# Optimization experiments

Hardware: AMD Instinct MI355X
Metric: run time of the kernel (lower is better)

## Reference

```python
import jax, jax.numpy as jnp
import numpy as np

B, N, DE, DH, L, DC = 8, 256, 768, 192, 2, 192
NEG = 1e30  # mask_logic constant from the repo


def setup_inputs() -> dict:
    ks = iter(jax.random.split(jax.random.key(0), 32))

    def nrm(shape, s=0.02):
        return jax.random.normal(next(ks), shape, dtype=jnp.float32) * s

    features = jax.random.normal(next(ks), (B, N, DE), dtype=jnp.float32)
    # DAG adjacency: node i attends to a subset of j < i; guarantee edge (i, i-1)
    rnd = jax.random.bernoulli(next(ks), 0.3, (B, N, N))
    tril = jnp.tril(jnp.ones((N, N), jnp.bool_), -1)
    adj = ((rnd & tril[None]) | jnp.eye(N, k=-1, dtype=jnp.bool_)[None]).astype(jnp.float32)
    s_mask = jax.random.bernoulli(next(ks), 0.5, (B, N, N)).astype(jnp.float32)
    s_mask_onehot = jnp.stack([1.0 - s_mask, s_mask], axis=-1)  # unused in forward
    lengths = jnp.full((B,), N, dtype=jnp.int32)  # unused (nodal_att_type=None)
    return dict(
        features=features, adj=adj, s_mask=s_mask,
        s_mask_onehot=s_mask_onehot, lengths=lengths,
        fc1_w=nrm((DE, DH)), fc1_b=jnp.zeros((DH,), jnp.float32),
        gat_w=nrm((L, 2 * DH)), gat_b=jnp.zeros((L,), jnp.float32),
        wr0=nrm((L, DH, DH)), wr1=nrm((L, DH, DH)),
        gruc_wih=nrm((L, 3 * DH, DH)), gruc_whh=nrm((L, 3 * DH, DH)),
        gruc_bih=jnp.zeros((L, 3 * DH), jnp.float32),
        gruc_bhh=jnp.zeros((L, 3 * DH), jnp.float32),
        grup_wih=nrm((L, 3 * DH, DH)), grup_whh=nrm((L, 3 * DH, DH)),
        grup_bih=jnp.zeros((L, 3 * DH), jnp.float32),
        grup_bhh=jnp.zeros((L, 3 * DH), jnp.float32),
        mlp_w0=nrm((DH * (L + 1), DH)), mlp_b0=jnp.zeros((DH,), jnp.float32),
        mlp_w1=nrm((DH, DH)), mlp_b1=jnp.zeros((DH,), jnp.float32),
        mlp_w2=nrm((DH, DC)), mlp_b2=jnp.zeros((DC,), jnp.float32),
    )


def _gru(x, h, wih, whh, bih, bhh):
    # torch.nn.GRUCell math
    gi = x @ wih.T + bih
    gh = h @ whh.T + bhh
    ir, iz, inn = jnp.split(gi, 3, axis=-1)
    hr, hz, hn = jnp.split(gh, 3, axis=-1)
    r = jax.nn.sigmoid(ir + hr)
    z = jax.nn.sigmoid(iz + hz)
    n = jnp.tanh(inn + r * hn)
    return (1.0 - z) * n + z * h


def _layer(Hl, adj, s_mask, gat_w, gat_b, wr0, wr1, cw, cp):
    # One DAG layer: sequential scan over nodes. Carry holds the relation-
    # projected value buffers V0=H1@Wr0^T, V1=H1@Wr1^T and per-node key
    # scores Ksc=H1@wk (rows >= i are zero and masked out), which is
    # mathematically identical to the torch code that re-projects the
    # growing H1 every step.
    wq, wk = gat_w[:DH], gat_w[DH:]
    pos = jnp.arange(N)

    def step(carry, xs):
        V0, V1, Ksc = carry
        i, x_i, adj_i, sm_i = xs  # x_i:(B,DH) adj_i,sm_i:(B,N)
        score = (x_i @ wq)[:, None] + Ksc + gat_b          # (B,N)
        mask = (pos < i)[None, :] & (adj_i > 0.5)          # ragged :i slice
        alpha = jnp.where(mask, score, score - NEG)        # mask_logic
        attn = jax.nn.softmax(alpha, axis=-1)              # masked -> exactly 0
        Vrel = V0 * sm_i[..., None] + V1 * (1.0 - sm_i[..., None])
        M = jnp.einsum('bn,bnd->bd', attn, Vrel)
        M = jnp.where(i > 0, M, 0.0)                       # node 0: no context
        C = _gru(x_i, M, *cw)
        P = _gru(M, x_i, *cp)
        Hnew = C + P
        V0 = V0.at[:, i, :].set(Hnew @ wr0.T)
        V1 = V1.at[:, i, :].set(Hnew @ wr1.T)
        Ksc = Ksc.at[:, i].set(Hnew @ wk)
        attn_out = jnp.where(i > 0, attn, 0.0)             # adjB row 0 is zeros
        return (V0, V1, Ksc), (Hnew, attn_out)

    z3 = jnp.zeros((B, N, DH), jnp.float32)
    carry0 = (z3, z3, jnp.zeros((B, N), jnp.float32))
    xs = (pos, Hl.transpose(1, 0, 2), adj.transpose(1, 0, 2), s_mask.transpose(1, 0, 2))
    _, (Hseq, Aseq) = jax.lax.scan(step, carry0, xs)
    return Hseq.transpose(1, 0, 2), Aseq.transpose(1, 0, 2)  # (B,N,DH),(B,N,N)


def reference(features, adj, s_mask, s_mask_onehot, lengths,
              fc1_w, fc1_b, gat_w, gat_b, wr0, wr1,
              gruc_wih, gruc_whh, gruc_bih, gruc_bhh,
              grup_wih, grup_whh, grup_bih, grup_bhh,
              mlp_w0, mlp_b0, mlp_w1, mlp_b1, mlp_w2, mlp_b2):
    Hl = jax.nn.relu(features @ fc1_w + fc1_b)  # H0
    Hs, As = [Hl], []
    for l in range(L):
        cw = (gruc_wih[l], gruc_whh[l], gruc_bih[l], gruc_bhh[l])
        cp = (grup_wih[l], grup_whh[l], grup_bih[l], grup_bhh[l])
        Hl, Al = _layer(Hl, adj, s_mask, gat_w[l], gat_b[l], wr0[l], wr1[l], cw, cp)
        Hs.append(Hl)
        As.append(Al)
    H = jnp.concatenate(Hs, axis=2)  # (B,N,DH*(L+1))
    # nodal_att_type=None => attentive_node_features is identity
    h = jax.nn.relu(H @ mlp_w0 + mlp_b0)
    h = jax.nn.relu(h @ mlp_w1 + mlp_b1)  # mlp_layers-1 = 1 extra block
    logits = h @ mlp_w2 + mlp_b2          # dropout: eval-mode identity
    return logits, jnp.stack(As, axis=1)  # (B,N,DC), (B,L,N,N)
```

## Files before the change

kernel.cpp:

```cpp
#include <hip/hip_runtime.h>
#include <stdint.h>

#define B_  8
#define N_  256
#define DH_ 192
#define L_  2
#define G3  576
#define G6  1152
#define NW  4
#define DS  48
#define KD  24
#define GC  288
#define MPSZ (8 * NW * DH_ * 3)
#define KDSZ (8 * NW)
#define STH 10001
#define STP 20001
#define SPK 50000
#define SF1 50001
#define SF2 50002
#define SDN 60001

typedef unsigned long long u64;

__device__ __forceinline__ float bflo(uint32_t u) { return __uint_as_float(u << 16); }
__device__ __forceinline__ float bfhi(uint32_t u) { return __uint_as_float(u & 0xffff0000u); }
__device__ __forceinline__ uint32_t f2bf(float f) {
    uint32_t x = __float_as_uint(f);
    x += 0x7fffu + ((x >> 16) & 1u);
    return x >> 16;
}
__device__ __forceinline__ float sigm(float x)  { return 1.f / (1.f + __expf(-x)); }
__device__ __forceinline__ float tanhf_(float x){ return 1.f - 2.f / (1.f + __expf(2.f * x)); }
__device__ __forceinline__ u64 packvs(float v, int st) {
    return ((u64)(uint32_t)st << 32) | __float_as_uint(v);
}
__device__ __forceinline__ u64 agload(const u64* p) {
    return __hip_atomic_load(p, __ATOMIC_RELAXED, __HIP_MEMORY_SCOPE_AGENT);
}
__device__ __forceinline__ void agstore(u64* p, u64 v) {
    __hip_atomic_store(p, v, __ATOMIC_RELAXED, __HIP_MEMORY_SCOPE_AGENT);
}
__device__ __forceinline__ float u2f(u64 v) { return __uint_as_float((uint32_t)v); }

__device__ __forceinline__ void wg_barrier() {
    asm volatile("s_waitcnt lgkmcnt(0)" ::: "memory");
    __builtin_amdgcn_s_barrier();
    asm volatile("" ::: "memory");
}

struct ScanSm {
    uint4 Wr4s[12 * DH_];
    float sA0[2][N_], sA1[2][N_], sKsc[N_];
    float sAdjN[N_], sSmN[N_];
    float sPre[6 * DS], sXv[DS];
    float sM[DH_], su0[DS], su1[DS], sGc[GC], sHn[DS];
    float sRl[DH_], sP0l[DH_], sP1l[DH_];
    float sRedS[2][8], sSaved[8], sSavedA[2], sSavedS[2];
};
struct WorkSm {
    float sX[DH_];
    float sPv[GC];
};
struct PrologSm {
    float sA[8][768];
    float sRed[3][8][192];
};
struct MlpSm {
    float sH[8][576];
    float sRed[3][8][192];
    float sT[8][192];
};
union SmemAll { ScanSm s; WorkSm w; PrologSm p; MlpSm m; };

__device__ void prepack_slice(int idx,
    const float* __restrict__ wr0, const float* __restrict__ wr1,
    const float* __restrict__ c_wih, const float* __restrict__ c_whh,
    const float* __restrict__ c_bih, const float* __restrict__ c_bhh,
    const float* __restrict__ p_wih, const float* __restrict__ p_whh,
    const float* __restrict__ p_bih, const float* __restrict__ p_bhh,
    float* __restrict__ WpreT, uint32_t* __restrict__ W4,
    uint32_t* __restrict__ Wr4, uint32_t* __restrict__ Wp4w,
    float* __restrict__ biasPre, float* __restrict__ gbx)
{
    for (int l = 0; l < L_; ++l) {
        const float* cwih = c_wih + l * G3 * DH_;
        const float* cwhh = c_whh + l * G3 * DH_;
        const float* pwih = p_wih + l * G3 * DH_;
        const float* pwhh = p_whh + l * G3 * DH_;
        if (l == 0) {
            int k = idx / G6, r = idx - k * G6;
            float w = (r < G3) ? cwih[r * DH_ + k] : pwhh[(r - G3) * DH_ + k];
            WpreT[k * G6 + r] = w;
        }
        if (idx < NW * 27648) {
            int w = idx / 27648, pos = idx % 27648;
            int p4 = pos / 1152, rem = pos % 1152;
            int c2 = rem >> 2, s = rem & 3;
            int p = 4 * p4 + s;
            int j = c2 / DS, dd = c2 % DS;
            int c = 192 * j + DS * w + dd;
            float w0 = (c < G3) ? cwhh[c * DH_ + 2 * p]     : pwih[(c - G3) * DH_ + 2 * p];
            float w1 = (c < G3) ? cwhh[c * DH_ + 2 * p + 1] : pwih[(c - G3) * DH_ + 2 * p + 1];
            W4[l * NW * 27648 + idx] = f2bf(w0) | (f2bf(w1) << 16);
            if (l == 1) {
                int r = c;
                float v0 = (r < G3) ? cwih[r * DH_ + 2 * p]     : pwhh[(r - G3) * DH_ + 2 * p];
                float v1 = (r < G3) ? cwih[r * DH_ + 2 * p + 1] : pwhh[(r - G3) * DH_ + 2 * p + 1];
                Wp4w[idx] = f2bf(v0) | (f2bf(v1) << 16);
            }
        }
        if (idx < NW * 9216) {
            int w = idx / 9216, pos = idx % 9216;
            int kq = pos / 768, rem = pos % 768;
            int d = rem >> 2, s = rem & 3;
            int k = DS * w + 4 * kq + s;
            Wr4[l * NW * 9216 + idx] =
                f2bf(wr0[l * DH_ * DH_ + d * DH_ + k]) |
                (f2bf(wr1[l * DH_ * DH_ + d * DH_ + k]) << 16);
        }
        if (idx < G6) {
            float base = (idx < G3) ? c_bih[l * G3 + idx] : p_bhh[l * G3 + idx - G3];
            float fold = 0.f;
            if (idx < 384)                    fold = c_bhh[l * G3 + idx];
            else if (idx >= G3 && idx < 960)  fold = p_bih[l * G3 + idx - G3];
            biasPre[l * G6 + idx] = base + fold;
        }
        if (idx < 384) {
            gbx[l * 384 + idx] = (idx < DH_) ? c_bhh[l * G3 + 384 + idx]
                                             : p_bih[l * G3 + 384 + (idx - DH_)];
        }
    }
}

__device__ void flag_sync(u64* flags, int wgid, int t, int stamp)
{
    __threadfence();
    __syncthreads();
    if (t == 0) agstore(&flags[wgid], packvs(0.f, stamp));
    if (t < 96) {
        while ((uint32_t)(agload(&flags[t]) >> 32) != (uint32_t)stamp) {}
    }
    __syncthreads();
    __threadfence();
    __syncthreads();
}

__device__ void prologue(char* smem, int wgid, int t,
    const float* __restrict__ features, const float* __restrict__ fc1_w,
    const float* __restrict__ fc1_b, const float* __restrict__ WpreT,
    const float* __restrict__ biasPre,
    float* __restrict__ Hcat, float* __restrict__ PREg, u64* __restrict__ Fp)
{
    PrologSm* P = (PrologSm*)smem;
    const int c = t % 192, kg = t / 192;
    for (int tt = wgid; tt < 256; tt += 96) {
        const int r0 = tt * 8;
        for (int q = t; q < 1536; q += 576) {
            int r = q / 192, c4 = q % 192;
            *(float4*)&P->sA[r][4 * c4] = *(const float4*)(features + (size_t)(r0 + r) * 768 + 4 * c4);
        }
        __syncthreads();
        {
            const float* bp = fc1_w + (size_t)(kg * 256) * 192 + c;
            float acc[8] = {0.f, 0.f, 0.f, 0.f, 0.f, 0.f, 0.f, 0.f};
            #pragma unroll 8
            for (int kk = 0; kk < 256; ++kk) {
                float bv = bp[(size_t)kk * 192];
                #pragma unroll
                for (int rr = 0; rr < 8; ++rr) acc[rr] += P->sA[rr][kg * 256 + kk] * bv;
            }
            #pragma unroll
            for (int rr = 0; rr < 8; ++rr) P->sRed[kg][rr][c] = acc[rr];
        }
        __syncthreads();
        if (t < 192) {
            float bv = fc1_b[t];
            #pragma unroll
            for (int rr = 0; rr < 8; ++rr) {
                float v = P->sRed[0][rr][t] + P->sRed[1][rr][t] + P->sRed[2][rr][t] + bv;
                Hcat[(size_t)(r0 + rr) * G3 + t] = fmaxf(v, 0.f);
            }
        }
        __syncthreads();
    }
    flag_sync(Fp + 96, wgid, t, SF1);
    {
        const float bpa = biasPre[t], bpb = biasPre[576 + t];
        for (int tt = wgid; tt < 256; tt += 96) {
            const int r0 = tt * 8;
            for (int q = t; q < 384; q += 576) {
                int r = q / 48, c4 = q % 48;
                *(float4*)&P->sA[r][4 * c4] = *(const float4*)(Hcat + (size_t)(r0 + r) * G3 + 4 * c4);
            }
            __syncthreads();
            {
                const float* b0 = WpreT + t;
                float a0[8] = {0.f,0.f,0.f,0.f,0.f,0.f,0.f,0.f};
                float a1[8] = {0.f,0.f,0.f,0.f,0.f,0.f,0.f,0.f};
                #pragma unroll 4
                for (int k = 0; k < 192; ++k) {
                    float bva = b0[(size_t)k * G6];
                    float bvb = b0[(size_t)k * G6 + 576];
                    #pragma unroll
                    for (int rr = 0; rr < 8; ++rr) {
                        float av = P->sA[rr][k];
                        a0[rr] += av * bva; a1[rr] += av * bvb;
                    }
                }
                #pragma unroll
                for (int rr = 0; rr < 8; ++rr) {
                    PREg[(size_t)(r0 + rr) * G6 + t]       = a0[rr] + bpa;
                    PREg[(size_t)(r0 + rr) * G6 + 576 + t] = a1[rr] + bpb;
                }
            }
            __syncthreads();
        }
    }
    flag_sync(Fp + 192, wgid, t, SF2);
}

__device__ void mlp_tail(char* smem, int wgid, int t,
    const float* __restrict__ Hcat,
    const float* __restrict__ mw0, const float* __restrict__ mb0,
    const float* __restrict__ mw1, const float* __restrict__ mb1,
    const float* __restrict__ mw2, const float* __restrict__ mb2,
    float* __restrict__ out, u64* __restrict__ Fd)
{
    if (t < 64) {
        while ((uint32_t)(agload(&Fd[t]) >> 32) != (uint32_t)SDN)
            __builtin_amdgcn_s_sleep(2);
    }
    __syncthreads();
    __threadfence();
    __syncthreads();
    MlpSm* M = (MlpSm*)smem;
    const int c = t % 192, kg = t / 192;
    for (int tt = wgid; tt < 256; tt += 96) {
        const int r0 = tt * 8;
        for (int q = t; q < 1152; q += 576) {
            int r = q / 144, c4 = q % 144;
            *(float4*)&M->sH[r][4 * c4] = *(const float4*)(Hcat + (size_t)(r0 + r) * G3 + 4 * c4);
        }
        __syncthreads();
        {
            const float* bp = mw0 + (size_t)(kg * 192) * 192 + c;
            float acc[8] = {0.f,0.f,0.f,0.f,0.f,0.f,0.f,0.f};
            #pragma unroll 8
            for (int kk = 0; kk < 192; ++kk) {
                float bv = bp[(size_t)kk * 192];
                #pragma unroll
                for (int rr = 0; rr < 8; ++rr) acc[rr] += M->sH[rr][kg * 192 + kk] * bv;
            }
            #pragma unroll
            for (int rr = 0; rr < 8; ++rr) M->sRed[kg][rr][c] = acc[rr];
        }
        __syncthreads();
        if (t < 192) {
            float bv = mb0[t];
            #pragma unroll
            for (int rr = 0; rr < 8; ++rr)
                M->sT[rr][t] = fmaxf(M->sRed[0][rr][t] + M->sRed[1][rr][t] + M->sRed[2][rr][t] + bv, 0.f);
        }
        __syncthreads();
        {
            const float* bp = mw1 + (size_t)(kg * 64) * 192 + c;
            float acc[8] = {0.f,0.f,0.f,0.f,0.f,0.f,0.f,0.f};
            #pragma unroll 8
            for (int kk = 0; kk < 64; ++kk) {
                float bv = bp[(size_t)kk * 192];
                #pragma unroll
                for (int rr = 0; rr < 8; ++rr) acc[rr] += M->sT[rr][kg * 64 + kk] * bv;
            }
            #pragma unroll
            for (int rr = 0; rr < 8; ++rr) M->sRed[kg][rr][c] = acc[rr];
        }
        __syncthreads();
        if (t < 192) {
            float bv = mb1[t];
            #pragma unroll
            for (int rr = 0; rr < 8; ++rr)
                M->sH[rr][t] = fmaxf(M->sRed[0][rr][t] + M->sRed[1][rr][t] + M->sRed[2][rr][t] + bv, 0.f);
        }
        __syncthreads();
        {
            const float* bp = mw2 + (size_t)(kg * 64) * 192 + c;
            float acc[8] = {0.f,0.f,0.f,0.f,0.f,0.f,0.f,0.f};
            #pragma unroll 8
            for (int kk = 0; kk < 64; ++kk) {
                float bv = bp[(size_t)kk * 192];
                #pragma unroll
                for (int rr = 0; rr < 8; ++rr) acc[rr] += M->sH[rr][kg * 64 + kk] * bv;
            }
            #pragma unroll
            for (int rr = 0; rr < 8; ++rr) M->sRed[kg][rr][c] = acc[rr];
        }
        __syncthreads();
        if (t < 192) {
            float bv = mb2[t];
            #pragma unroll
            for (int rr = 0; rr < 8; ++rr)
                out[(size_t)(r0 + rr) * 192 + t] =
                    M->sRed[0][rr][t] + M->sRed[1][rr][t] + M->sRed[2][rr][t] + bv;
        }
        __syncthreads();
    }
}

template<int ISL2>
__device__ void scan_body(
    ScanSm* S, int b, int w, int t,
    const float* __restrict__ xin, float* __restrict__ hout,
    const float* __restrict__ PREg, const float* __restrict__ adj,
    const float* __restrict__ smask,
    const uint32_t* __restrict__ W4l, const uint32_t* __restrict__ Wr4l,
    const float* __restrict__ gbxl, const float* __restrict__ gatwl,
    uint32_t* __restrict__ Hw, u64* __restrict__ MPsl, u64* __restrict__ Kdl,
    u64* __restrict__ HcW, const u64* __restrict__ HcR,
    const u64* __restrict__ PREcR,
    float* __restrict__ AsB, int sbase)
{
    const int lane = t & 63, wave = t >> 6;
    const int dg0 = w * DS;
    const float* adjB = adj   + (size_t)b * N_ * N_;
    const float* smB  = smask + (size_t)b * N_ * N_;
    const int fi = b * NW;
    const int cB4 = t >> 1, khB4 = t & 1;
    const int w1 = (w + 1) & 3, w2 = (w + 2) & 3, w3 = (w + 3) & 3;

    {
        uint32_t* wr = (uint32_t*)S->Wr4s;
        for (int q = t; q < 9216; q += 576) wr[q] = Wr4l[q];
    }
    uint4 wreg[12];
    {
        const uint4* W4v = (const uint4*)W4l;
        #pragma unroll
        for (int p4 = 0; p4 < 12; ++p4) wreg[p4] = W4v[(12 * khB4 + p4) * GC + cB4];
    }
    float wkv = 0.f, g2b = 0.f, g5b = 0.f;
    if (t < DS) { wkv = gatwl[DH_ + dg0 + t]; g2b = gbxl[dg0 + t]; g5b = gbxl[DH_ + dg0 + t]; }
    if (t < N_) { S->sKsc[t] = 0.f; S->sA0[1][t] = 0.f; S->sA1[1][t] = 0.f; }
    if (t < DS) { S->su0[t] = 0.f; S->su1[t] = 0.f; }
    if (t < 8)  S->sRedS[1][t] = 0.f;
    if (w == 0 && t < N_) AsB[t] = 0.f;

    if (!ISL2) {
        if (t < DS) {
            const float* pre = PREg + (size_t)(b * N_) * G6 + dg0 + t;
            S->sPre[t] = pre[0]; S->sPre[DS + t] = pre[192]; S->sPre[2 * DS + t] = pre[384];
            S->sPre[3 * DS + t] = pre[576]; S->sPre[4 * DS + t] = pre[768]; S->sPre[5 * DS + t] = pre[960];
            S->sXv[t] = xin[(size_t)(b * N_) * G3 + dg0 + t];
        }
        for (int q = t; q < 128; q += 576) {
            if (q < 64)  *(float4*)&S->sAdjN[4 * q] = *(const float4*)(adjB + N_ + 4 * q);
            else { int q2 = q - 64; *(float4*)&S->sSmN[4 * q2] = *(const float4*)(smB + N_ + 4 * q2); }
        }
    } else {
        for (int q = t; q < 320; q += 576) {
            if (q < 64)       *(float4*)&S->sAdjN[4 * q] = *(const float4*)(adjB + N_ + 4 * q);
            else if (q < 128) { int q2 = q - 64;  *(float4*)&S->sSmN[4 * q2] = *(const float4*)(smB + N_ + 4 * q2); }
            else if (q < 176) {
                int d = q - 128;
                const u64* p = HcR + ((size_t)(b * N_) * NW + w) * DS + d;
                u64 v; do { v = agload(p); } while ((uint32_t)(v >> 32) != (uint32_t)STH);
                S->sXv[d] = __uint_as_float((uint32_t)v);
            } else {
                int qq = q - 176;
                const u64* p = PREcR + ((size_t)(b * N_) * NW + w) * 144 + qq;
                u64 v; do { v = agload(p); } while ((uint32_t)(v >> 32) != (uint32_t)STP);
                uint32_t pl = (uint32_t)v;
                S->sPre[2 * qq] = bflo(pl); S->sPre[2 * qq + 1] = bfhi(pl);
            }
        }
    }
    __syncthreads();
    {
        float hn = 0.f;
        if (t < DS) {
            float xv = S->sXv[t];
            float r1 = sigm(S->sPre[t]), z1 = sigm(S->sPre[DS + t]);
            float n1 = tanhf_(S->sPre[2 * DS + t] + r1 * g2b);
            float Cv = (1.f - z1) * n1;
            float r2 = sigm(S->sPre[3 * DS + t]), z2 = sigm(S->sPre[4 * DS + t]);
            float n2 = tanhf_(g5b + r2 * S->sPre[5 * DS + t]);
            hn = Cv + (1.f - z2) * n2 + z2 * xv;
            S->sHn[t] = hn;
            hout[(size_t)(b * N_) * G3 + dg0 + t] = hn;
            if (!ISL2) HcW[((size_t)(b * N_) * NW + w) * DS + t] = packvs(hn, STH);
        }
        if (t == 0) { S->sSavedA[1] = S->sAdjN[0]; S->sSavedS[1] = S->sSmN[0]; }
        if (wave == 0) {
            float v = hn * wkv;
            #pragma unroll
            for (int o = 32; o; o >>= 1) v += __shfl_xor(v, o);
            if (lane == 0) { S->sSaved[6] = v; agstore(&Kdl[fi + w], packvs(v, sbase)); }
        }
    }
    __syncthreads();
    if (t < KD) Hw[(size_t)t * N_] = f2bf(S->sHn[2 * t]) | (f2bf(S->sHn[2 * t + 1]) << 16);
    __syncthreads();

    for (int i = 1; i < N_; ++i) {
        const int row = b * N_ + i;
        const int stamp = sbase + i;
        const int pp = i & 1, pn = pp ^ 1;

        if (t < DH_) {
            float rr = 0.f, p0 = 0.f, p1 = 0.f;
            #pragma unroll 4
            for (int kq = 0; kq < 12; ++kq) {
                uint4 wv = S->Wr4s[kq * DH_ + t];
                const int k0 = 4 * kq;
                float lo, hi;
                lo = bflo(wv.x); hi = bfhi(wv.x);
                rr = fmaf(S->su0[k0 + 0], lo, rr); rr = fmaf(S->su1[k0 + 0], hi, rr);
                p0 = fmaf(S->sHn[k0 + 0], lo, p0); p1 = fmaf(S->sHn[k0 + 0], hi, p1);
                lo = bflo(wv.y); hi = bfhi(wv.y);
                rr = fmaf(S->su0[k0 + 1], lo, rr); rr = fmaf(S->su1[k0 + 1], hi, rr);
                p0 = fmaf(S->sHn[k0 + 1], lo, p0); p1 = fmaf(S->sHn[k0 + 1], hi, p1);
                lo = bflo(wv.z); hi = bfhi(wv.z);
                rr = fmaf(S->su0[k0 + 2], lo, rr); rr = fmaf(S->su1[k0 + 2], hi, rr);
                p0 = fmaf(S->sHn[k0 + 2], lo, p0); p1 = fmaf(S->sHn[k0 + 2], hi, p1);
                lo = bflo(wv.w); hi = bfhi(wv.w);
                rr = fmaf(S->su0[k0 + 3], lo, rr); rr = fmaf(S->su1[k0 + 3], hi, rr);
                p0 = fmaf(S->sHn[k0 + 3], lo, p0); p1 = fmaf(S->sHn[k0 + 3], hi, p1);
            }
            S->sRl[t] = rr; S->sP0l[t] = p0; S->sP1l[t] = p1;
            u64* base = &MPsl[(size_t)pp * MPSZ + ((size_t)(fi + w) * DH_ + t) * 3];
            agstore(base + 0, packvs(rr, stamp));
            agstore(base + 1, packvs(p0, stamp));
            agstore(base + 2, packvs(p1, stamp));
        } else if (t >= 384) {
            const int u = t - 384;
            const int inx = (i + 1 < N_) ? i + 1 : N_ - 1;
            if (!ISL2) {
                for (int qq = u; qq < 212; qq += 192) {
                    if (qq < 64)
                        *(float4*)&S->sAdjN[4 * qq] = *(const float4*)(adjB + (size_t)inx * N_ + 4 * qq);
                    else if (qq < 128) { int q2 = qq - 64;
                        *(float4*)&S->sSmN[4 * q2] = *(const float4*)(smB + (size_t)inx * N_ + 4 * q2); }
                    else if (qq < 140) { int q2 = qq - 128;
                        *(float4*)&S->sXv[4 * q2] = *(const float4*)(xin + (size_t)row * G3 + dg0 + 4 * q2); }
                    else { int q2 = qq - 140; int g = q2 / 12, o = q2 - 12 * g;
                        *(float4*)&S->sPre[g * DS + 4 * o] =
                            *(const float4*)(PREg + (size_t)row * G6 + g * DH_ + dg0 + 4 * o); }
                }
            } else {
                for (int qq = u; qq < 320; qq += 192) {
                    if (qq < 64)
                        *(float4*)&S->sAdjN[4 * qq] = *(const float4*)(adjB + (size_t)inx * N_ + 4 * qq);
                    else if (qq < 128) { int q2 = qq - 64;
                        *(float4*)&S->sSmN[4 * q2] = *(const float4*)(smB + (size_t)inx * N_ + 4 * q2); }
                    else if (qq < 176) {
                        int d = qq - 128;
                        const u64* p = HcR + ((size_t)row * NW + w) * DS + d;
                        u64 v; do { v = agload(p); } while ((uint32_t)(v >> 32) != (uint32_t)(STH + i));
                        S->sXv[d] = __uint_as_float((uint32_t)v);
                    } else {
                        int q2 = qq - 176;
                        const u64* p = PREcR + ((size_t)row * NW + w) * 144 + q2;
                        u64 v; do { v = agload(p); } while ((uint32_t)(v >> 32) != (uint32_t)(STP + i));
                        uint32_t pl = (uint32_t)v;
                        S->sPre[2 * q2] = bflo(pl); S->sPre[2 * q2 + 1] = bfhi(pl);
                    }
                }
            }
        }
        wg_barrier();

        if (t < N_) {
            float e = 0.f;
            if (t == i) { S->sSavedA[pn] = S->sAdjN[t]; S->sSavedS[pn] = S->sSmN[t]; }
            if (t < i - 1 && S->sAdjN[t] > 0.5f) e = __expf(S->sKsc[t]);
            float b0 = e * S->sSmN[t];
            S->sA0[pn][t] = b0; S->sA1[pn][t] = e - b0;
            float ps = e;
            #pragma unroll
            for (int o = 32; o; o >>= 1) ps += __shfl_xor(ps, o);
            if (lane == 0) S->sRedS[pn][wave] = ps;
        }
        wg_barrier();

        if (t < 384) {
            const int ilim = i - 1;
            const int kd = t >> 4, jp = t & 15;
            const uint32_t* hp = Hw + (size_t)kd * N_;
            float u0l = 0.f, u0h = 0.f, u1l = 0.f, u1h = 0.f;
            int j = jp;
            while (j + 48 < ilim) {
                uint32_t h0 = hp[j], h1 = hp[j + 16], h2 = hp[j + 32], h3 = hp[j + 48];
                float b0, b1;
                b0 = S->sA0[pn][j];      b1 = S->sA1[pn][j];
                u0l = fmaf(b0, bflo(h0), u0l); u0h = fmaf(b0, bfhi(h0), u0h);
                u1l = fmaf(b1, bflo(h0), u1l); u1h = fmaf(b1, bfhi(h0), u1h);
                b0 = S->sA0[pn][j + 16]; b1 = S->sA1[pn][j + 16];
                u0l = fmaf(b0, bflo(h1), u0l); u0h = fmaf(b0, bfhi(h1), u0h);
                u1l = fmaf(b1, bflo(h1), u1l); u1h = fmaf(b1, bfhi(h1), u1h);
                b0 = S->sA0[pn][j + 32]; b1 = S->sA1[pn][j + 32];
                u0l = fmaf(b0, bflo(h2), u0l); u0h = fmaf(b0, bfhi(h2), u0h);
                u1l = fmaf(b1, bflo(h2), u1l); u1h = fmaf(b1, bfhi(h2), u1h);
                b0 = S->sA0[pn][j + 48]; b1 = S->sA1[pn][j + 48];
                u0l = fmaf(b0, bflo(h3), u0l); u0h = fmaf(b0, bfhi(h3), u0h);
                u1l = fmaf(b1, bflo(h3), u1l); u1h = fmaf(b1, bfhi(h3), u1h);
                j += 64;
            }
            for (; j < ilim; j += 16) {
                uint32_t hv = hp[j];
                float b0 = S->sA0[pn][j], b1 = S->sA1[pn][j];
                u0l = fmaf(b0, bflo(hv), u0l); u0h = fmaf(b0, bfhi(hv), u0h);
                u1l = fmaf(b1, bflo(hv), u1l); u1h = fmaf(b1, bfhi(hv), u1h);
            }
            #pragma unroll
            for (int o = 1; o <= 8; o <<= 1) {
                u0l += __shfl_xor(u0l, o); u0h += __shfl_xor(u0h, o);
                u1l += __shfl_xor(u1l, o); u1h += __shfl_xor(u1h, o);
            }
            if (jp == 0) {
                S->su0[2 * kd] = u0l; S->su0[2 * kd + 1] = u0h;
                S->su1[2 * kd] = u1l; S->su1[2 * kd + 1] = u1h;
            }
        } else {
            const int d = t - 384;
            const u64* pA = &MPsl[(size_t)pp * MPSZ + ((size_t)(fi + w1) * DH_ + d) * 3];
            const u64* pB = &MPsl[(size_t)pp * MPSZ + ((size_t)(fi + w2) * DH_ + d) * 3];
            const u64* pC = &MPsl[(size_t)pp * MPSZ + ((size_t)(fi + w3) * DH_ + d) * 3];
            const uint32_t ex = (uint32_t)stamp;
            u64 a0, a1, a2, b0, b1, b2, c0, c1, c2;
            do {
                a0 = agload(pA); a1 = agload(pA + 1); a2 = agload(pA + 2);
                b0 = agload(pB); b1 = agload(pB + 1); b2 = agload(pB + 2);
                c0 = agload(pC); c1 = agload(pC + 1); c2 = agload(pC + 2);
            } while ((uint32_t)(a0 >> 32) != ex || (uint32_t)(a1 >> 32) != ex ||
                     (uint32_t)(a2 >> 32) != ex || (uint32_t)(b0 >> 32) != ex ||
                     (uint32_t)(b1 >> 32) != ex || (uint32_t)(b2 >> 32) != ex ||
                     (uint32_t)(c0 >> 32) != ex || (uint32_t)(c1 >> 32) != ex ||
                     (uint32_t)(c2 >> 32) != ex);
            S->sRl[d]  += u2f(a0) + u2f(b0) + u2f(c0);
            S->sP0l[d] += u2f(a1) + u2f(b1) + u2f(c1);
            S->sP1l[d] += u2f(a2) + u2f(b2) + u2f(c2);
            if (t == 575) {
                const uint32_t ex2 = (uint32_t)(stamp - 1);
                const int kpar = (i - 1) & 1;
                u64 k0, k1, k2;
                u64* q1 = &Kdl[kpar * KDSZ + fi + w1];
                u64* q2 = &Kdl[kpar * KDSZ + fi + w2];
                u64* q3 = &Kdl[kpar * KDSZ + fi + w3];
                do {
                    k0 = agload(q1); k1 = agload(q2); k2 = agload(q3);
                } while ((uint32_t)(k0 >> 32) != ex2 || (uint32_t)(k1 >> 32) != ex2 ||
                         (uint32_t)(k2 >> 32) != ex2);
                float kdot = S->sSaved[6] + u2f(k0) + u2f(k1) + u2f(k2);
                float adj1 = S->sSavedA[pp], sm1 = S->sSavedS[pp];
                float er = __expf(kdot);
                float e1 = (adj1 > 0.5f) ? er : 0.f;
                float Ssum = S->sRedS[pp][0] + S->sRedS[pp][1] + S->sRedS[pp][2]
                           + S->sRedS[pp][3] + S->sRedS[pp][4] + e1;
                S->sKsc[i - 1] = kdot;
                float invS = 1.f / Ssum;
                float e1c0 = e1 * sm1, e1c1 = e1 - e1c0;
                S->sSaved[2] = invS;
                S->sSaved[4] = e1c0; S->sSaved[5] = e1c1;
                S->sA0[pp][i - 1] = e1c0; S->sA1[pp][i - 1] = e1c1;
                float adjn = S->sAdjN[i - 1], smn = S->sSmN[i - 1];
                float en = (adjn > 0.5f) ? er : 0.f;
                float n0 = en * smn;
                S->sA0[pn][i - 1] = n0; S->sA1[pn][i - 1] = en - n0;
                S->sRedS[pn][4] = en;
            }
        }
        wg_barrier();

        if (t < DH_) {
            S->sM[t] = (S->sRl[t] + S->sSaved[4] * S->sP0l[t]
                                  + S->sSaved[5] * S->sP1l[t]) * S->sSaved[2];
        } else if (t < 192 + DS) {
            const int k = t - 192;
            float a0 = S->sA0[pn][i - 1], a1 = S->sA1[pn][i - 1];
            S->su0[k] += a0 * S->sHn[k];
            S->su1[k] += a1 * S->sHn[k];
        } else if (w == 0 && t >= 256 && t < 512) {
            const int j = t - 256;
            AsB[(size_t)i * N_ + j] = (S->sA0[pp][j] + S->sA1[pp][j]) * S->sSaved[2];
        }
        wg_barrier();

        {
            float g = 0.f;
            #pragma unroll
            for (int p4 = 0; p4 < 12; ++p4) {
                const uint4 wv = wreg[p4];
                const int m0 = 8 * (12 * khB4 + p4);
                g = fmaf(S->sM[m0 + 0], bflo(wv.x), g); g = fmaf(S->sM[m0 + 1], bfhi(wv.x), g);
                g = fmaf(S->sM[m0 + 2], bflo(wv.y), g); g = fmaf(S->sM[m0 + 3], bfhi(wv.y), g);
                g = fmaf(S->sM[m0 + 4], bflo(wv.z), g); g = fmaf(S->sM[m0 + 5], bfhi(wv.z), g);
                g = fmaf(S->sM[m0 + 6], bflo(wv.w), g); g = fmaf(S->sM[m0 + 7], bfhi(wv.w), g);
            }
            g += __shfl_xor(g, 1);
            if (khB4 == 0) S->sGc[cB4] = g;
        }
        wg_barrier();

        {
            float hn = 0.f;
            if (t < DS) {
                float Mv = S->sM[dg0 + t];
                float r1 = sigm(S->sPre[t] + S->sGc[t]);
                float z1 = sigm(S->sPre[DS + t] + S->sGc[DS + t]);
                float n1 = tanhf_(S->sPre[2 * DS + t] + r1 * (S->sGc[2 * DS + t] + g2b));
                float Cv = (1.f - z1) * n1 + z1 * Mv;
                float r2 = sigm(S->sGc[3 * DS + t] + S->sPre[3 * DS + t]);
                float z2 = sigm(S->sGc[4 * DS + t] + S->sPre[4 * DS + t]);
                float n2 = tanhf_(S->sGc[5 * DS + t] + g5b + r2 * S->sPre[5 * DS + t]);
                hn = Cv + (1.f - z2) * n2 + z2 * S->sXv[t];
                S->sHn[t] = hn;
                hout[(size_t)row * G3 + dg0 + t] = hn;
                if (!ISL2) HcW[((size_t)row * NW + w) * DS + t] = packvs(hn, STH + i);
            }
            if (wave == 0) {
                float v = hn * wkv;
                #pragma unroll
                for (int o = 32; o; o >>= 1) v += __shfl_xor(v, o);
                if (lane == 0) { S->sSaved[6] = v; agstore(&Kdl[pp * KDSZ + fi + w], packvs(v, stamp)); }
            }
            if (t < KD) Hw[(size_t)t * N_ + i] = f2bf(S->sHn[2 * t]) | (f2bf(S->sHn[2 * t + 1]) << 16);
        }
        wg_barrier();
    }
}

__device__ void worker_body(WorkSm* Wm, int b, int w, int t,
    const uint32_t* __restrict__ Wp4g, const float* __restrict__ bias2,
    const u64* __restrict__ HcR, u64* __restrict__ PREcW)
{
    const int c = t >> 1, kh = t & 1;
    uint4 wpreg[12];
    {
        const uint4* v4 = (const uint4*)Wp4g;
        #pragma unroll
        for (int p4 = 0; p4 < 12; ++p4) wpreg[p4] = v4[(12 * kh + p4) * GC + c];
    }
    float bv = 0.f;
    if (kh == 0) bv = bias2[192 * (c / DS) + w * DS + (c % DS)];
    for (int i = 0; i < N_; ++i) {
        if (t < DH_) {
            const u64* p = HcR + ((size_t)(b * N_ + i) * NW + (t / DS)) * DS + (t % DS);
            u64 v; do { v = agload(p); } while ((uint32_t)(v >> 32) != (uint32_t)(STH + i));
            Wm->sX[t] = __uint_as_float((uint32_t)v);
        }
        wg_barrier();
        {
            float g = 0.f;
            #pragma unroll
            for (int p4 = 0; p4 < 12; ++p4) {
                const uint4 wv = wpreg[p4];
                const int m0 = 8 * (12 * kh + p4);
                g = fmaf(Wm->sX[m0 + 0], bflo(wv.x), g); g = fmaf(Wm->sX[m0 + 1], bfhi(wv.x), g);
                g = fmaf(Wm->sX[m0 + 2], bflo(wv.y), g); g = fmaf(Wm->sX[m0 + 3], bfhi(wv.y), g);
                g = fmaf(Wm->sX[m0 + 4], bflo(wv.z), g); g = fmaf(Wm->sX[m0 + 5], bfhi(wv.z), g);
                g = fmaf(Wm->sX[m0 + 6], bflo(wv.w), g); g = fmaf(Wm->sX[m0 + 7], bfhi(wv.w), g);
            }
            g += __shfl_xor(g, 1);
            if (kh == 0) Wm->sPv[c] = g + bv;
        }
        wg_barrier();
        if (t < 144) {
            u64 v = ((u64)(uint32_t)(STP + i) << 32)
                  | f2bf(Wm->sPv[2 * t]) | (f2bf(Wm->sPv[2 * t + 1]) << 16);
            agstore(&PREcW[((size_t)(b * N_ + i) * NW + w) * 144 + t], v);
        }
        wg_barrier();
    }
}

__global__ __launch_bounds__(576, 1) void pipeline_kernel(
    const float* __restrict__ features, const float* __restrict__ fc1_w,
    const float* __restrict__ fc1_b,
    const float* __restrict__ adj, const float* __restrict__ smask,
    const float* __restrict__ gatw,
    const float* __restrict__ wr0, const float* __restrict__ wr1,
    const float* __restrict__ c_wih, const float* __restrict__ c_whh,
    const float* __restrict__ c_bih, const float* __restrict__ c_bhh,
    const float* __restrict__ p_wih, const float* __restrict__ p_whh,
    const float* __restrict__ p_bih, const float* __restrict__ p_bhh,
    const float* __restrict__ mw0, const float* __restrict__ mb0,
    const float* __restrict__ mw1, const float* __restrict__ mb1,
    const float* __restrict__ mw2, const float* __restrict__ mb2,
    float* __restrict__ Hcat, float* __restrict__ PREg,
    float* __restrict__ WpreT, uint32_t* __restrict__ W4,
    uint32_t* __restrict__ Wr4, uint32_t* __restrict__ Wp4w,
    float* __restrict__ biasPre, float* __restrict__ gbx,
    uint32_t* __restrict__ Hb, u64* __restrict__ MPs, u64* __restrict__ Kd,
    u64* __restrict__ Hc, u64* __restrict__ PREc,
    u64* __restrict__ Fp, u64* __restrict__ Fd,
    float* __restrict__ out)
{
    __shared__ __align__(16) char smem[sizeof(SmemAll)];
    const int blk = blockIdx.x, t = threadIdx.x;
    const int wgid = blk;
    const int b = blk & 7, r12 = blk >> 3;
    const int role = r12 >> 2, w = r12 & 3;

    for (int j = 0; j < 4; ++j) {
        int idx = wgid * 576 + t + 55296 * j;
        prepack_slice(idx, wr0, wr1, c_wih, c_whh, c_bih, c_bhh,
                      p_wih, p_whh, p_bih, p_bhh,
                      WpreT, W4, Wr4, Wp4w, biasPre, gbx);
    }
    flag_sync(Fp, wgid, t, SPK);

    prologue(smem, wgid, t, features, fc1_w, fc1_b, WpreT, biasPre,
             Hcat, PREg, Fp);

    float* As = out + 393216;
    if (role == 0) {
        scan_body<0>((ScanSm*)smem, b, w, t,
            Hcat, Hcat + 192, PREg, adj, smask,
            W4, Wr4, gbx, gatw,
            Hb + (size_t)(b * NW + w) * KD * N_, MPs, Kd,
            Hc, nullptr, nullptr,
            As + (size_t)b * (L_ * N_ * N_), 1);
        __threadfence();
        __syncthreads();
        if (t == 0) agstore(&Fd[b * 8 + w], packvs(0.f, SDN));
    } else if (role == 2) {
        scan_body<1>((ScanSm*)smem, b, w, t,
            nullptr, Hcat + 384, nullptr, adj, smask,
            W4 + NW * 27648, Wr4 + NW * 9216, gbx + 384, gatw + 384,
            Hb + (size_t)(32 + b * NW + w) * KD * N_,
            MPs + (size_t)2 * MPSZ, Kd + 2 * KDSZ,
            nullptr, Hc, PREc,
            As + (size_t)b * (L_ * N_ * N_) + N_ * N_, 30001);
        __threadfence();
        __syncthreads();
        if (t == 0) agstore(&Fd[b * 8 + 4 + w], packvs(0.f, SDN));
    } else {
        worker_body((WorkSm*)smem, b, w, t,
            Wp4w + (size_t)w * 27648, biasPre + G6,
            Hc, PREc);
    }

    mlp_tail(smem, wgid, t, Hcat, mw0, mb0, mw1, mb1, mw2, mb2, out, Fd);
}

extern "C" void kernel_launch(void* const* d_in, const int* in_sizes, int n_in,
                              void* d_out, int out_size, void* d_ws, size_t ws_size,
                              hipStream_t stream)
{
    const float* features = (const float*)d_in[0];
    const float* adj      = (const float*)d_in[1];
    const float* smask    = (const float*)d_in[2];
    const float* fc1_w = (const float*)d_in[5];
    const float* fc1_b = (const float*)d_in[6];
    const float* gat_w = (const float*)d_in[7];
    const float* wr0   = (const float*)d_in[9];
    const float* wr1   = (const float*)d_in[10];
    const float* c_wih = (const float*)d_in[11];
    const float* c_whh = (const float*)d_in[12];
    const float* c_bih = (const float*)d_in[13];
    const float* c_bhh = (const float*)d_in[14];
    const float* p_wih = (const float*)d_in[15];
    const float* p_whh = (const float*)d_in[16];
    const float* p_bih = (const float*)d_in[17];
    const float* p_bhh = (const float*)d_in[18];
    const float* mw0 = (const float*)d_in[19];
    const float* mb0 = (const float*)d_in[20];
    const float* mw1 = (const float*)d_in[21];
    const float* mb1 = (const float*)d_in[22];
    const float* mw2 = (const float*)d_in[23];
    const float* mb2 = (const float*)d_in[24];
    float* out = (float*)d_out;

    char* wsb = (char*)d_ws;
    size_t off = 0;
    auto carve = [&](size_t bytes) -> char* {
        char* p = wsb + off;
        off = (off + bytes + 255) & ~(size_t)255;
        return p;
    };
    float* Hcat     = (float*)carve(2048ull * 576 * 4);
    float* PREg     = (float*)carve(2048ull * 1152 * 4);
    float* WpreT    = (float*)carve(192ull * 1152 * 4);
    uint32_t* W4    = (uint32_t*)carve(2ull * NW * 27648 * 4);
    uint32_t* Wr4   = (uint32_t*)carve(2ull * NW * 9216 * 4);
    uint32_t* Wp4w  = (uint32_t*)carve((size_t)NW * 27648 * 4);
    float* biasPre  = (float*)carve(2ull * 1152 * 4);
    float* gbx      = (float*)carve(2ull * 384 * 4);
    uint32_t* Hb    = (uint32_t*)carve(64ull * KD * 256 * 4);
    u64* MPs        = (u64*)carve(4ull * MPSZ * 8);
    u64* Kd         = (u64*)carve(4ull * KDSZ * 8);
    u64* Hc         = (u64*)carve(8ull * 256 * NW * DS * 8);
    u64* PREc       = (u64*)carve(8ull * 256 * NW * 144 * 8);
    u64* Fp         = (u64*)carve(288ull * 8);
    u64* Fd         = (u64*)carve(64ull * 8);

    pipeline_kernel<<<dim3(96), 576, 0, stream>>>(
        features, fc1_w, fc1_b, adj, smask, gat_w,
        wr0, wr1, c_wih, c_whh, c_bih, c_bhh, p_wih, p_whh, p_bih, p_bhh,
        mw0, mb0, mw1, mb1, mw2, mb2,
        Hcat, PREg, WpreT, W4, Wr4, Wp4w, biasPre, gbx,
        Hb, MPs, Kd, Hc, PREc, Fp, Fd, out);
}
```

Baseline: 1.652 ms.

## Split each layer scan over two workgroups instead of four per batch

Each batch's sequential DAG scan now runs on 2 workgroups, each owning 96 hidden dims, instead of 4 owning 48. Each scan workgroup keeps its full GRU hidden-weight slice in registers, one column per thread, so the cross-thread shuffle reduction goes away. Every step now waits on one peer's partial relation projections and key dots instead of three, cutting cross-workgroup spin-wait traffic on the latency-bound serial path. In exchange each workgroup does twice the per-step arithmetic and register pressure rises; the launch-bounds hint also changes and idle workgroups appear.

```diff
diff --git a/kernel.cpp b/kernel.cpp
--- a/kernel.cpp
+++ b/kernel.cpp
@@ -5,14 +5,15 @@
 #define N_  256
 #define DH_ 192
 #define L_  2
+#define NS  2
+#define NWK 4
+#define DS  96
+#define KD  48
+#define GC  576
 #define G3  576
 #define G6  1152
-#define NW  4
-#define DS  48
-#define KD  24
-#define GC  288
-#define MPSZ (8 * NW * DH_ * 3)
-#define KDSZ (8 * NW)
+#define MPSZ (8 * NS * DH_ * 3)
+#define KDSZ (8 * NS * 2)
 #define STH 10001
 #define STP 20001
 #define SPK 50000
@@ -49,8 +50,9 @@
 }
 
 struct ScanSm {
-    uint4 Wr4s[12 * DH_];
-    float sA0[2][N_], sA1[2][N_], sKsc[N_];
+    uint4 wrS4[24 * DH_];
+    float sA0[2][N_], sA1[2][N_];
+    float sKsc[N_];
     float sAdjN[N_], sSmN[N_];
     float sPre[6 * DS], sXv[DS];
     float sM[DH_], su0[DS], su1[DS], sGc[GC], sHn[DS];
@@ -59,7 +61,7 @@
 };
 struct WorkSm {
     float sX[DH_];
-    float sPv[GC];
+    float sPv[288];
 };
 struct PrologSm {
     float sA[8][768];
@@ -82,53 +84,58 @@
     uint32_t* __restrict__ Wr4, uint32_t* __restrict__ Wp4w,
     float* __restrict__ biasPre, float* __restrict__ gbx)
 {
-    for (int l = 0; l < L_; ++l) {
-        const float* cwih = c_wih + l * G3 * DH_;
-        const float* cwhh = c_whh + l * G3 * DH_;
-        const float* pwih = p_wih + l * G3 * DH_;
-        const float* pwhh = p_whh + l * G3 * DH_;
-        if (l == 0) {
-            int k = idx / G6, r = idx - k * G6;
-            float w = (r < G3) ? cwih[r * DH_ + k] : pwhh[(r - G3) * DH_ + k];
-            WpreT[k * G6 + r] = w;
-        }
-        if (idx < NW * 27648) {
-            int w = idx / 27648, pos = idx % 27648;
-            int p4 = pos / 1152, rem = pos % 1152;
-            int c2 = rem >> 2, s = rem & 3;
-            int p = 4 * p4 + s;
-            int j = c2 / DS, dd = c2 % DS;
-            int c = 192 * j + DS * w + dd;
-            float w0 = (c < G3) ? cwhh[c * DH_ + 2 * p]     : pwih[(c - G3) * DH_ + 2 * p];
-            float w1 = (c < G3) ? cwhh[c * DH_ + 2 * p + 1] : pwih[(c - G3) * DH_ + 2 * p + 1];
-            W4[l * NW * 27648 + idx] = f2bf(w0) | (f2bf(w1) << 16);
-            if (l == 1) {
-                int r = c;
-                float v0 = (r < G3) ? cwih[r * DH_ + 2 * p]     : pwhh[(r - G3) * DH_ + 2 * p];
-                float v1 = (r < G3) ? cwih[r * DH_ + 2 * p + 1] : pwhh[(r - G3) * DH_ + 2 * p + 1];
-                Wp4w[idx] = f2bf(v0) | (f2bf(v1) << 16);
-            }
-        }
-        if (idx < NW * 9216) {
-            int w = idx / 9216, pos = idx % 9216;
-            int kq = pos / 768, rem = pos % 768;
-            int d = rem >> 2, s = rem & 3;
-            int k = DS * w + 4 * kq + s;
-            Wr4[l * NW * 9216 + idx] =
+    {
+        int k = idx / G6, r = idx - k * G6;
+        float w = (r < G3) ? c_wih[r * DH_ + k] : p_whh[(r - G3) * DH_ + k];
+        WpreT[k * G6 + r] = w;
+    }
+    {
+        int l = idx / 110592, o = idx - l * 110592;
+        int w = o / 55296, o2 = o - w * 55296;
+        int c2 = o2 / 96, ku = o2 - c2 * 96;
+        int j = c2 / 96, dd = c2 - j * 96;
+        int gc = 192 * j + 96 * w + dd;
+        const float* W = (gc < G3) ? (c_whh + (size_t)(l * G3 + gc) * DH_)
+                                   : (p_wih + (size_t)(l * G3 + gc - G3) * DH_);
+        W4[idx] = f2bf(W[2 * ku]) | (f2bf(W[2 * ku + 1]) << 16);
+    }
+    if (idx < NWK * 27648) {
+        int w = idx / 27648, pos = idx % 27648;
+        int p4 = pos / 1152, rem = pos % 1152;
+        int c2 = rem >> 2, s = rem & 3;
+        int p = 4 * p4 + s;
+        int j = c2 / 48, dd = c2 % 48;
+        int c = 192 * j + 48 * w + dd;
+        const float* W = (c < G3) ? (c_wih + (size_t)(G3 + c) * DH_)
+                                  : (p_whh + (size_t)(G3 + c - G3) * DH_);
+        Wp4w[idx] = f2bf(W[2 * p]) | (f2bf(W[2 * p + 1]) << 16);
+    }
+    if (idx < 36864) {
+        int w = idx / 18432, pos = idx % 18432;
+        int kq = pos / 768, rem = pos % 768;
+        int d = rem >> 2, s = rem & 3;
+        int k = 96 * w + 4 * kq + s;
+        #pragma unroll
+        for (int l = 0; l < L_; ++l)
+            Wr4[l * 36864 + idx] =
                 f2bf(wr0[l * DH_ * DH_ + d * DH_ + k]) |
                 (f2bf(wr1[l * DH_ * DH_ + d * DH_ + k]) << 16);
-        }
-        if (idx < G6) {
+    }
+    if (idx < G6) {
+        #pragma unroll
+        for (int l = 0; l < L_; ++l) {
             float base = (idx < G3) ? c_bih[l * G3 + idx] : p_bhh[l * G3 + idx - G3];
             float fold = 0.f;
             if (idx < 384)                    fold = c_bhh[l * G3 + idx];
             else if (idx >= G3 && idx < 960)  fold = p_bih[l * G3 + idx - G3];
             biasPre[l * G6 + idx] = base + fold;
         }
-        if (idx < 384) {
+    }
+    if (idx < 384) {
+        #pragma unroll
+        for (int l = 0; l < L_; ++l)
             gbx[l * 384 + idx] = (idx < DH_) ? c_bhh[l * G3 + 384 + idx]
                                              : p_bih[l * G3 + 384 + (idx - DH_)];
-        }
     }
 }
 
@@ -226,7 +233,7 @@
     const float* __restrict__ mw2, const float* __restrict__ mb2,
     float* __restrict__ out, u64* __restrict__ Fd)
 {
-    if (t < 64) {
+    if (t < 32) {
         while ((uint32_t)(agload(&Fd[t]) >> 32) != (uint32_t)SDN)
             __builtin_amdgcn_s_sleep(2);
     }
@@ -312,7 +319,8 @@
     const float* __restrict__ xin, float* __restrict__ hout,
     const float* __restrict__ PREg, const float* __restrict__ adj,
     const float* __restrict__ smask,
-    const uint32_t* __restrict__ W4l, const uint32_t* __restrict__ Wr4l,
+    const uint32_t* __restrict__ W4l,
+    const uint32_t* __restrict__ Wr4l,
     const float* __restrict__ gbxl, const float* __restrict__ gatwl,
     uint32_t* __restrict__ Hw, u64* __restrict__ MPsl, u64* __restrict__ Kdl,
     u64* __restrict__ HcW, const u64* __restrict__ HcR,
@@ -321,21 +329,20 @@
 {
     const int lane = t & 63, wave = t >> 6;
     const int dg0 = w * DS;
+    const int ws = w ^ 1;
     const float* adjB = adj   + (size_t)b * N_ * N_;
     const float* smB  = smask + (size_t)b * N_ * N_;
-    const int fi = b * NW;
-    const int cB4 = t >> 1, khB4 = t & 1;
-    const int w1 = (w + 1) & 3, w2 = (w + 2) & 3, w3 = (w + 3) & 3;
+    const int fi = b * NS;
 
     {
-        uint32_t* wr = (uint32_t*)S->Wr4s;
-        for (int q = t; q < 9216; q += 576) wr[q] = Wr4l[q];
-    }
-    uint4 wreg[12];
+        uint32_t* wr = (uint32_t*)S->wrS4;
+        for (int q = t; q < 18432; q += 576) wr[q] = Wr4l[q];
+    }
+    uint4 wfreg[24];
     {
-        const uint4* W4v = (const uint4*)W4l;
+        const uint4* wf4 = (const uint4*)(W4l + (size_t)w * 55296);
         #pragma unroll
-        for (int p4 = 0; p4 < 12; ++p4) wreg[p4] = W4v[(12 * khB4 + p4) * GC + cB4];
+        for (int p4 = 0; p4 < 24; ++p4) wfreg[p4] = wf4[t * 24 + p4];
     }
     float wkv = 0.f, g2b = 0.f, g5b = 0.f;
     if (t < DS) { wkv = gatwl[DH_ + dg0 + t]; g2b = gbxl[dg0 + t]; g5b = gbxl[DH_ + dg0 + t]; }
@@ -356,20 +363,22 @@
             else { int q2 = q - 64; *(float4*)&S->sSmN[4 * q2] = *(const float4*)(smB + N_ + 4 * q2); }
         }
     } else {
-        for (int q = t; q < 320; q += 576) {
+        for (int q = t; q < 512; q += 576) {
             if (q < 64)       *(float4*)&S->sAdjN[4 * q] = *(const float4*)(adjB + N_ + 4 * q);
             else if (q < 128) { int q2 = q - 64;  *(float4*)&S->sSmN[4 * q2] = *(const float4*)(smB + N_ + 4 * q2); }
-            else if (q < 176) {
+            else if (q < 224) {
                 int d = q - 128;
-                const u64* p = HcR + ((size_t)(b * N_) * NW + w) * DS + d;
+                const u64* p = HcR + (size_t)(b * N_) * DH_ + dg0 + d;
                 u64 v; do { v = agload(p); } while ((uint32_t)(v >> 32) != (uint32_t)STH);
                 S->sXv[d] = __uint_as_float((uint32_t)v);
             } else {
-                int qq = q - 176;
-                const u64* p = PREcR + ((size_t)(b * N_) * NW + w) * 144 + qq;
+                int q2 = q - 224;
+                int h = q2 / 144, qi = q2 % 144;
+                const u64* p = PREcR + ((size_t)(b * N_) * NWK + 2 * w + h) * 144 + qi;
                 u64 v; do { v = agload(p); } while ((uint32_t)(v >> 32) != (uint32_t)STP);
                 uint32_t pl = (uint32_t)v;
-                S->sPre[2 * qq] = bflo(pl); S->sPre[2 * qq + 1] = bfhi(pl);
+                int g = qi / 24, dd = (2 * qi) % 48, dl = 48 * h + dd;
+                S->sPre[g * DS + dl] = bflo(pl); S->sPre[g * DS + dl + 1] = bfhi(pl);
             }
         }
     }
@@ -386,14 +395,17 @@
             hn = Cv + (1.f - z2) * n2 + z2 * xv;
             S->sHn[t] = hn;
             hout[(size_t)(b * N_) * G3 + dg0 + t] = hn;
-            if (!ISL2) HcW[((size_t)(b * N_) * NW + w) * DS + t] = packvs(hn, STH);
+            if (!ISL2) HcW[(size_t)(b * N_) * DH_ + dg0 + t] = packvs(hn, STH);
         }
         if (t == 0) { S->sSavedA[1] = S->sAdjN[0]; S->sSavedS[1] = S->sSmN[0]; }
-        if (wave == 0) {
-            float v = hn * wkv;
+        if (wave < 2) {
+            float v = (t < DS) ? hn * wkv : 0.f;
             #pragma unroll
             for (int o = 32; o; o >>= 1) v += __shfl_xor(v, o);
-            if (lane == 0) { S->sSaved[6] = v; agstore(&Kdl[fi + w], packvs(v, sbase)); }
+            if (lane == 0) {
+                S->sSaved[6 + wave] = v;
+                agstore(&Kdl[(fi + w) * 2 + wave], packvs(v, sbase));
+            }
         }
     }
     __syncthreads();
@@ -408,8 +420,8 @@
         if (t < DH_) {
             float rr = 0.f, p0 = 0.f, p1 = 0.f;
             #pragma unroll 4
-            for (int kq = 0; kq < 12; ++kq) {
-                uint4 wv = S->Wr4s[kq * DH_ + t];
+            for (int kq = 0; kq < 24; ++kq) {
+                uint4 wv = S->wrS4[kq * DH_ + t];
                 const int k0 = 4 * kq;
                 float lo, hi;
                 lo = bflo(wv.x); hi = bfhi(wv.x);
@@ -430,38 +442,43 @@
             agstore(base + 0, packvs(rr, stamp));
             agstore(base + 1, packvs(p0, stamp));
             agstore(base + 2, packvs(p1, stamp));
+        } else if (t < 192 + KD) {
+            const int tt = t - 192;
+            Hw[(size_t)tt * N_ + (i - 1)] = f2bf(S->sHn[2 * tt]) | (f2bf(S->sHn[2 * tt + 1]) << 16);
         } else if (t >= 384) {
             const int u = t - 384;
             const int inx = (i + 1 < N_) ? i + 1 : N_ - 1;
             if (!ISL2) {
-                for (int qq = u; qq < 212; qq += 192) {
+                for (int qq = u; qq < 296; qq += 192) {
                     if (qq < 64)
                         *(float4*)&S->sAdjN[4 * qq] = *(const float4*)(adjB + (size_t)inx * N_ + 4 * qq);
                     else if (qq < 128) { int q2 = qq - 64;
                         *(float4*)&S->sSmN[4 * q2] = *(const float4*)(smB + (size_t)inx * N_ + 4 * q2); }
-                    else if (qq < 140) { int q2 = qq - 128;
+                    else if (qq < 152) { int q2 = qq - 128;
                         *(float4*)&S->sXv[4 * q2] = *(const float4*)(xin + (size_t)row * G3 + dg0 + 4 * q2); }
-                    else { int q2 = qq - 140; int g = q2 / 12, o = q2 - 12 * g;
+                    else { int q2 = qq - 152; int g = q2 / 24, o = q2 - 24 * g;
                         *(float4*)&S->sPre[g * DS + 4 * o] =
                             *(const float4*)(PREg + (size_t)row * G6 + g * DH_ + dg0 + 4 * o); }
                 }
             } else {
-                for (int qq = u; qq < 320; qq += 192) {
+                for (int qq = u; qq < 512; qq += 192) {
                     if (qq < 64)
                         *(float4*)&S->sAdjN[4 * qq] = *(const float4*)(adjB + (size_t)inx * N_ + 4 * qq);
                     else if (qq < 128) { int q2 = qq - 64;
                         *(float4*)&S->sSmN[4 * q2] = *(const float4*)(smB + (size_t)inx * N_ + 4 * q2); }
-                    else if (qq < 176) {
+                    else if (qq < 224) {
                         int d = qq - 128;
-                        const u64* p = HcR + ((size_t)row * NW + w) * DS + d;
+                        const u64* p = HcR + (size_t)row * DH_ + dg0 + d;
                         u64 v; do { v = agload(p); } while ((uint32_t)(v >> 32) != (uint32_t)(STH + i));
                         S->sXv[d] = __uint_as_float((uint32_t)v);
                     } else {
-                        int q2 = qq - 176;
-                        const u64* p = PREcR + ((size_t)row * NW + w) * 144 + q2;
+                        int q2 = qq - 224;
+                        int h = q2 / 144, qi = q2 % 144;
+                        const u64* p = PREcR + ((size_t)row * NWK + 2 * w + h) * 144 + qi;
                         u64 v; do { v = agload(p); } while ((uint32_t)(v >> 32) != (uint32_t)(STP + i));
                         uint32_t pl = (uint32_t)v;
-                        S->sPre[2 * q2] = bflo(pl); S->sPre[2 * q2 + 1] = bfhi(pl);
+                        int g = qi / 24, dd = (2 * qi) % 48, dl = 48 * h + dd;
+                        S->sPre[g * DS + dl] = bflo(pl); S->sPre[g * DS + dl + 1] = bfhi(pl);
                     }
                 }
             }
@@ -483,35 +500,35 @@
 
         if (t < 384) {
             const int ilim = i - 1;
-            const int kd = t >> 4, jp = t & 15;
+            const int kd = t >> 3, jp = t & 7;
             const uint32_t* hp = Hw + (size_t)kd * N_;
             float u0l = 0.f, u0h = 0.f, u1l = 0.f, u1h = 0.f;
             int j = jp;
-            while (j + 48 < ilim) {
-                uint32_t h0 = hp[j], h1 = hp[j + 16], h2 = hp[j + 32], h3 = hp[j + 48];
+            while (j + 24 < ilim) {
+                uint32_t h0 = hp[j], h1 = hp[j + 8], h2 = hp[j + 16], h3 = hp[j + 24];
                 float b0, b1;
                 b0 = S->sA0[pn][j];      b1 = S->sA1[pn][j];
                 u0l = fmaf(b0, bflo(h0), u0l); u0h = fmaf(b0, bfhi(h0), u0h);
                 u1l = fmaf(b1, bflo(h0), u1l); u1h = fmaf(b1, bfhi(h0), u1h);
-                b0 = S->sA0[pn][j + 16]; b1 = S->sA1[pn][j + 16];
+                b0 = S->sA0[pn][j + 8];  b1 = S->sA1[pn][j + 8];
                 u0l = fmaf(b0, bflo(h1), u0l); u0h = fmaf(b0, bfhi(h1), u0h);
                 u1l = fmaf(b1, bflo(h1), u1l); u1h = fmaf(b1, bfhi(h1), u1h);
-                b0 = S->sA0[pn][j + 32]; b1 = S->sA1[pn][j + 32];
+                b0 = S->sA0[pn][j + 16]; b1 = S->sA1[pn][j + 16];
                 u0l = fmaf(b0, bflo(h2), u0l); u0h = fmaf(b0, bfhi(h2), u0h);
                 u1l = fmaf(b1, bflo(h2), u1l); u1h = fmaf(b1, bfhi(h2), u1h);
-                b0 = S->sA0[pn][j + 48]; b1 = S->sA1[pn][j + 48];
+                b0 = S->sA0[pn][j + 24]; b1 = S->sA1[pn][j + 24];
                 u0l = fmaf(b0, bflo(h3), u0l); u0h = fmaf(b0, bfhi(h3), u0h);
                 u1l = fmaf(b1, bflo(h3), u1l); u1h = fmaf(b1, bfhi(h3), u1h);
-                j += 64;
-            }
-            for (; j < ilim; j += 16) {
+                j += 32;
+            }
+            for (; j < ilim; j += 8) {
                 uint32_t hv = hp[j];
                 float b0 = S->sA0[pn][j], b1 = S->sA1[pn][j];
                 u0l = fmaf(b0, bflo(hv), u0l); u0h = fmaf(b0, bfhi(hv), u0h);
                 u1l = fmaf(b1, bflo(hv), u1l); u1h = fmaf(b1, bfhi(hv), u1h);
             }
             #pragma unroll
-            for (int o = 1; o <= 8; o <<= 1) {
+            for (int o = 1; o <= 4; o <<= 1) {
                 u0l += __shfl_xor(u0l, o); u0h += __shfl_xor(u0h, o);
                 u1l += __shfl_xor(u1l, o); u1h += __shfl_xor(u1h, o);
             }
@@ -521,35 +538,26 @@
             }
         } else {
             const int d = t - 384;
-            const u64* pA = &MPsl[(size_t)pp * MPSZ + ((size_t)(fi + w1) * DH_ + d) * 3];
-            const u64* pB = &MPsl[(size_t)pp * MPSZ + ((size_t)(fi + w2) * DH_ + d) * 3];
-            const u64* pC = &MPsl[(size_t)pp * MPSZ + ((size_t)(fi + w3) * DH_ + d) * 3];
+            const u64* pA = &MPsl[(size_t)pp * MPSZ + ((size_t)(fi + ws) * DH_ + d) * 3];
             const uint32_t ex = (uint32_t)stamp;
-            u64 a0, a1, a2, b0, b1, b2, c0, c1, c2;
+            u64 a0, a1, a2;
             do {
                 a0 = agload(pA); a1 = agload(pA + 1); a2 = agload(pA + 2);
-                b0 = agload(pB); b1 = agload(pB + 1); b2 = agload(pB + 2);
-                c0 = agload(pC); c1 = agload(pC + 1); c2 = agload(pC + 2);
             } while ((uint32_t)(a0 >> 32) != ex || (uint32_t)(a1 >> 32) != ex ||
-                     (uint32_t)(a2 >> 32) != ex || (uint32_t)(b0 >> 32) != ex ||
-                     (uint32_t)(b1 >> 32) != ex || (uint32_t)(b2 >> 32) != ex ||
-                     (uint32_t)(c0 >> 32) != ex || (uint32_t)(c1 >> 32) != ex ||
-                     (uint32_t)(c2 >> 32) != ex);
-            S->sRl[d]  += u2f(a0) + u2f(b0) + u2f(c0);
-            S->sP0l[d] += u2f(a1) + u2f(b1) + u2f(c1);
-            S->sP1l[d] += u2f(a2) + u2f(b2) + u2f(c2);
+                     (uint32_t)(a2 >> 32) != ex);
+            S->sRl[d]  += u2f(a0);
+            S->sP0l[d] += u2f(a1);
+            S->sP1l[d] += u2f(a2);
             if (t == 575) {
                 const uint32_t ex2 = (uint32_t)(stamp - 1);
                 const int kpar = (i - 1) & 1;
-                u64 k0, k1, k2;
-                u64* q1 = &Kdl[kpar * KDSZ + fi + w1];
-                u64* q2 = &Kdl[kpar * KDSZ + fi + w2];
-                u64* q3 = &Kdl[kpar * KDSZ + fi + w3];
+                u64 k0, k1;
+                u64* q1 = &Kdl[kpar * KDSZ + (fi + ws) * 2 + 0];
+                u64* q2 = &Kdl[kpar * KDSZ + (fi + ws) * 2 + 1];
                 do {
-                    k0 = agload(q1); k1 = agload(q2); k2 = agload(q3);
-                } while ((uint32_t)(k0 >> 32) != ex2 || (uint32_t)(k1 >> 32) != ex2 ||
-                         (uint32_t)(k2 >> 32) != ex2);
-                float kdot = S->sSaved[6] + u2f(k0) + u2f(k1) + u2f(k2);
+                    k0 = agload(q1); k1 = agload(q2);
+                } while ((uint32_t)(k0 >> 32) != ex2 || (uint32_t)(k1 >> 32) != ex2);
+                float kdot = S->sSaved[6] + S->sSaved[7] + u2f(k0) + u2f(k1);
                 float adj1 = S->sSavedA[pp], sm1 = S->sSavedS[pp];
                 float er = __expf(kdot);
                 float e1 = (adj1 > 0.5f) ? er : 0.f;
@@ -578,8 +586,8 @@
             float a0 = S->sA0[pn][i - 1], a1 = S->sA1[pn][i - 1];
             S->su0[k] += a0 * S->sHn[k];
             S->su1[k] += a1 * S->sHn[k];
-        } else if (w == 0 && t >= 256 && t < 512) {
-            const int j = t - 256;
+        } else if (w == 0 && t >= 288 && t < 544) {
+            const int j = t - 288;
             AsB[(size_t)i * N_ + j] = (S->sA0[pp][j] + S->sA1[pp][j]) * S->sSaved[2];
         }
         wg_barrier();
@@ -587,16 +595,16 @@
         {
             float g = 0.f;
             #pragma unroll
-            for (int p4 = 0; p4 < 12; ++p4) {
-                const uint4 wv = wreg[p4];
-                const int m0 = 8 * (12 * khB4 + p4);
-                g = fmaf(S->sM[m0 + 0], bflo(wv.x), g); g = fmaf(S->sM[m0 + 1], bfhi(wv.x), g);
-                g = fmaf(S->sM[m0 + 2], bflo(wv.y), g); g = fmaf(S->sM[m0 + 3], bfhi(wv.y), g);
-                g = fmaf(S->sM[m0 + 4], bflo(wv.z), g); g = fmaf(S->sM[m0 + 5], bfhi(wv.z), g);
-                g = fmaf(S->sM[m0 + 6], bflo(wv.w), g); g = fmaf(S->sM[m0 + 7], bfhi(wv.w), g);
-            }
-            g += __shfl_xor(g, 1);
-            if (khB4 == 0) S->sGc[cB4] = g;
+            for (int p4 = 0; p4 < 24; ++p4) {
+                const uint4 wv = wfreg[p4];
+                const float4 ma = *(const float4*)&S->sM[8 * p4];
+                const float4 mb = *(const float4*)&S->sM[8 * p4 + 4];
+                g = fmaf(bflo(wv.x), ma.x, g); g = fmaf(bfhi(wv.x), ma.y, g);
+                g = fmaf(bflo(wv.y), ma.z, g); g = fmaf(bfhi(wv.y), ma.w, g);
+                g = fmaf(bflo(wv.z), mb.x, g); g = fmaf(bfhi(wv.z), mb.y, g);
+                g = fmaf(bflo(wv.w), mb.z, g); g = fmaf(bfhi(wv.w), mb.w, g);
+            }
+            S->sGc[t] = g;
         }
         wg_barrier();
 
@@ -614,15 +622,17 @@
                 hn = Cv + (1.f - z2) * n2 + z2 * S->sXv[t];
                 S->sHn[t] = hn;
                 hout[(size_t)row * G3 + dg0 + t] = hn;
-                if (!ISL2) HcW[((size_t)row * NW + w) * DS + t] = packvs(hn, STH + i);
-            }
-            if (wave == 0) {
-                float v = hn * wkv;
+                if (!ISL2) HcW[(size_t)row * DH_ + dg0 + t] = packvs(hn, STH + i);
+            }
+            if (wave < 2) {
+                float v = (t < DS) ? hn * wkv : 0.f;
                 #pragma unroll
                 for (int o = 32; o; o >>= 1) v += __shfl_xor(v, o);
-                if (lane == 0) { S->sSaved[6] = v; agstore(&Kdl[pp * KDSZ + fi + w], packvs(v, stamp)); }
-            }
-            if (t < KD) Hw[(size_t)t * N_ + i] = f2bf(S->sHn[2 * t]) | (f2bf(S->sHn[2 * t + 1]) << 16);
+                if (lane == 0) {
+                    S->sSaved[6 + wave] = v;
+                    agstore(&Kdl[pp * KDSZ + (fi + w) * 2 + wave], packvs(v, stamp));
+                }
+            }
         }
         wg_barrier();
     }
@@ -637,13 +647,13 @@
     {
         const uint4* v4 = (const uint4*)Wp4g;
         #pragma unroll
-        for (int p4 = 0; p4 < 12; ++p4) wpreg[p4] = v4[(12 * kh + p4) * GC + c];
+        for (int p4 = 0; p4 < 12; ++p4) wpreg[p4] = v4[(12 * kh + p4) * 288 + c];
     }
     float bv = 0.f;
-    if (kh == 0) bv = bias2[192 * (c / DS) + w * DS + (c % DS)];
+    if (kh == 0) bv = bias2[192 * (c / 48) + w * 48 + (c % 48)];
     for (int i = 0; i < N_; ++i) {
         if (t < DH_) {
-            const u64* p = HcR + ((size_t)(b * N_ + i) * NW + (t / DS)) * DS + (t % DS);
+            const u64* p = HcR + (size_t)(b * N_ + i) * DH_ + t;
             u64 v; do { v = agload(p); } while ((uint32_t)(v >> 32) != (uint32_t)(STH + i));
             Wm->sX[t] = __uint_as_float((uint32_t)v);
         }
@@ -666,13 +676,13 @@
         if (t < 144) {
             u64 v = ((u64)(uint32_t)(STP + i) << 32)
                   | f2bf(Wm->sPv[2 * t]) | (f2bf(Wm->sPv[2 * t + 1]) << 16);
-            agstore(&PREcW[((size_t)(b * N_ + i) * NW + w) * 144 + t], v);
+            agstore(&PREcW[((size_t)(b * N_ + i) * NWK + w) * 144 + t], v);
         }
         wg_barrier();
     }
 }
 
-__global__ __launch_bounds__(576, 1) void pipeline_kernel(
+__global__ __launch_bounds__(576, 3) void pipeline_kernel(
     const float* __restrict__ features, const float* __restrict__ fc1_w,
     const float* __restrict__ fc1_b,
     const float* __restrict__ adj, const float* __restrict__ smask,
@@ -696,50 +706,50 @@
 {
     __shared__ __align__(16) char smem[sizeof(SmemAll)];
     const int blk = blockIdx.x, t = threadIdx.x;
-    const int wgid = blk;
     const int b = blk & 7, r12 = blk >> 3;
-    const int role = r12 >> 2, w = r12 & 3;
 
     for (int j = 0; j < 4; ++j) {
-        int idx = wgid * 576 + t + 55296 * j;
+        int idx = blk * 576 + t + 55296 * j;
         prepack_slice(idx, wr0, wr1, c_wih, c_whh, c_bih, c_bhh,
                       p_wih, p_whh, p_bih, p_bhh,
                       WpreT, W4, Wr4, Wp4w, biasPre, gbx);
     }
-    flag_sync(Fp, wgid, t, SPK);
-
-    prologue(smem, wgid, t, features, fc1_w, fc1_b, WpreT, biasPre,
+    flag_sync(Fp, blk, t, SPK);
+
+    prologue(smem, blk, t, features, fc1_w, fc1_b, WpreT, biasPre,
              Hcat, PREg, Fp);
 
     float* As = out + 393216;
-    if (role == 0) {
+    if (r12 < 2) {
+        const int w = r12;
         scan_body<0>((ScanSm*)smem, b, w, t,
             Hcat, Hcat + 192, PREg, adj, smask,
-            W4, Wr4, gbx, gatw,
-            Hb + (size_t)(b * NW + w) * KD * N_, MPs, Kd,
+            W4, Wr4 + (size_t)w * 18432, gbx, gatw,
+            Hb + (size_t)(b * NS + w) * KD * N_, MPs, Kd,
             Hc, nullptr, nullptr,
             As + (size_t)b * (L_ * N_ * N_), 1);
         __threadfence();
         __syncthreads();
-        if (t == 0) agstore(&Fd[b * 8 + w], packvs(0.f, SDN));
-    } else if (role == 2) {
+        if (t == 0) agstore(&Fd[b * 4 + w], packvs(0.f, SDN));
+    } else if (r12 >= 6 && r12 < 8) {
+        const int w = r12 - 6;
         scan_body<1>((ScanSm*)smem, b, w, t,
             nullptr, Hcat + 384, nullptr, adj, smask,
-            W4 + NW * 27648, Wr4 + NW * 9216, gbx + 384, gatw + 384,
-            Hb + (size_t)(32 + b * NW + w) * KD * N_,
+            W4 + 110592, Wr4 + 36864 + (size_t)w * 18432, gbx + 384, gatw + 384,
+            Hb + (size_t)(16 + b * NS + w) * KD * N_,
             MPs + (size_t)2 * MPSZ, Kd + 2 * KDSZ,
             nullptr, Hc, PREc,
             As + (size_t)b * (L_ * N_ * N_) + N_ * N_, 30001);
         __threadfence();
         __syncthreads();
-        if (t == 0) agstore(&Fd[b * 8 + 4 + w], packvs(0.f, SDN));
-    } else {
-        worker_body((WorkSm*)smem, b, w, t,
-            Wp4w + (size_t)w * 27648, biasPre + G6,
+        if (t == 0) agstore(&Fd[b * 4 + 2 + w], packvs(0.f, SDN));
+    } else if (r12 < 6) {
+        worker_body((WorkSm*)smem, b, r12 - 2, t,
+            Wp4w + (size_t)(r12 - 2) * 27648, biasPre + G6,
             Hc, PREc);
     }
 
-    mlp_tail(smem, wgid, t, Hcat, mw0, mb0, mw1, mb1, mw2, mb2, out, Fd);
+    mlp_tail(smem, blk, t, Hcat, mw0, mb0, mw1, mb1, mw2, mb2, out, Fd);
 }
 
 extern "C" void kernel_launch(void* const* d_in, const int* in_sizes, int n_in,
@@ -779,17 +789,17 @@
     };
     float* Hcat     = (float*)carve(2048ull * 576 * 4);
     float* PREg     = (float*)carve(2048ull * 1152 * 4);
-    float* WpreT    = (float*)carve(192ull * 1152 * 4);
-    uint32_t* W4    = (uint32_t*)carve(2ull * NW * 27648 * 4);
-    uint32_t* Wr4   = (uint32_t*)carve(2ull * NW * 9216 * 4);
-    uint32_t* Wp4w  = (uint32_t*)carve((size_t)NW * 27648 * 4);
-    float* biasPre  = (float*)carve(2ull * 1152 * 4);
-    float* gbx      = (float*)carve(2ull * 384 * 4);
-    uint32_t* Hb    = (uint32_t*)carve(64ull * KD * 256 * 4);
+    float* WpreT    = (float*)carve(221184ull * 4);
+    uint32_t* W4    = (uint32_t*)carve(221184ull * 4);
+    uint32_t* Wr4   = (uint32_t*)carve(73728ull * 4);
+    uint32_t* Wp4w  = (uint32_t*)carve(110592ull * 4);
+    float* biasPre  = (float*)carve(2304ull * 4);
+    float* gbx      = (float*)carve(768ull * 4);
+    uint32_t* Hb    = (uint32_t*)carve(32ull * KD * 256 * 4);
     u64* MPs        = (u64*)carve(4ull * MPSZ * 8);
     u64* Kd         = (u64*)carve(4ull * KDSZ * 8);
-    u64* Hc         = (u64*)carve(8ull * 256 * NW * DS * 8);
-    u64* PREc       = (u64*)carve(8ull * 256 * NW * 144 * 8);
+    u64* Hc         = (u64*)carve(2048ull * 192 * 8);
+    u64* PREc       = (u64*)carve(2048ull * 576 * 8);
     u64* Fp         = (u64*)carve(288ull * 8);
     u64* Fd         = (u64*)carve(64ull * 8);
 
```

New measurement: 4.294 ms. +159.9%, slower.
